# Optimization experiments

Hardware: AMD Instinct MI355X
Metric: run time of the kernel (lower is better)

## Reference

```python
import jax, jax.numpy as jnp
import numpy as np

VOCAB = 32000
EMB = 1024
SEQ = 2048
STACK = 8
N_HEADS = 16
ATTN = 64
BATCH = 2


def _ln(x, g, b, eps=1e-5):
    mu = jnp.mean(x, axis=-1, keepdims=True)
    var = jnp.var(x, axis=-1, keepdims=True)
    return (x - mu) * jax.lax.rsqrt(var + eps) * g + b


def setup_inputs() -> dict:
    key = jax.random.key(0)
    ks = jax.random.split(key, 16)
    s = lambda *sh: 0.02
    inp = {
        "x": jax.random.randint(ks[0], (BATCH, SEQ), 0, VOCAB),
        "emb": jax.random.normal(ks[1], (VOCAB, EMB), jnp.float32) * 0.02,
        # NOTE: one shared Attention_Head (all n_heads identical) and one shared Decoder (all stack layers identical)
        "Wq": jax.random.normal(ks[2], (EMB, ATTN), jnp.float32) * 0.02,
        "bq": jnp.zeros((ATTN,), jnp.float32),
        "Wk": jax.random.normal(ks[3], (EMB, ATTN), jnp.float32) * 0.02,
        "bk": jnp.zeros((ATTN,), jnp.float32),
        "Wv": jax.random.normal(ks[4], (EMB, ATTN), jnp.float32) * 0.02,
        "bv": jnp.zeros((ATTN,), jnp.float32),
        "Wd": jax.random.normal(ks[5], (ATTN * N_HEADS, EMB), jnp.float32) * 0.02,
        "bd": jnp.zeros((EMB,), jnp.float32),
        "g1": jnp.ones((EMB,), jnp.float32),
        "beta1": jnp.zeros((EMB,), jnp.float32),
        "g2": jnp.ones((EMB,), jnp.float32),
        "beta2": jnp.zeros((EMB,), jnp.float32),
        "W1": jax.random.normal(ks[6], (EMB, 4 * EMB), jnp.float32) * 0.02,
        "c1": jnp.zeros((4 * EMB,), jnp.float32),
        "W2": jax.random.normal(ks[7], (4 * EMB, EMB), jnp.float32) * 0.02,
        "c2": jnp.zeros((EMB,), jnp.float32),
        "Wfc": jax.random.normal(ks[8], (EMB, VOCAB), jnp.float32) * 0.02,
        "bfc": jnp.zeros((VOCAB,), jnp.float32),
    }
    return inp


def reference(x, emb, Wq, bq, Wk, bk, Wv, bv, Wd, bd, g1, beta1, g2, beta2, W1, c1, W2, c2, Wfc, bfc):
    h = emb[x]  # [B, S, E]
    scale = ATTN ** (-0.5)
    for _ in range(STACK):  # same (shared) decoder params every layer
        z = _ln(h, g1, beta1)
        q = z @ Wq + bq  # [B,S,A]
        k = z @ Wk + bk
        v = z @ Wv + bv
        # no causal mask applied in the original (tril buffer is unused)
        attn = jax.nn.softmax(jnp.einsum("bqa,bka->bqk", q, k) * scale, axis=-1)
        head = attn @ v  # [B,S,A]; all heads share weights -> identical outputs
        cat = jnp.tile(head, (1, 1, N_HEADS))  # [B,S,A*H]
        h = h + cat @ Wd + bd
        z2 = _ln(h, g2, beta2)
        h = h + jax.nn.relu(z2 @ W1 + c1) @ W2 + c2
    return h @ Wfc + bfc  # [B,S,VOCAB]
```

## Files before the change

kernel.cpp:

```cpp
#include <hip/hip_runtime.h>

typedef unsigned short u16;
typedef __attribute__((ext_vector_type(4))) float f32x4;
typedef __attribute__((ext_vector_type(8))) __bf16 bf16x8;
typedef __attribute__((ext_vector_type(4))) unsigned short u16x4;

static __device__ __forceinline__ u16 f2bf(float f) {
  union { float f; unsigned u; } v; v.f = f;
  unsigned r = v.u + 0x7fffu + ((v.u >> 16) & 1u);
  return (u16)(r >> 16);
}

#define GLD_LDS(g, l) __builtin_amdgcn_global_load_lds( \
    (const __attribute__((address_space(1))) void*)(g), \
    (__attribute__((address_space(3))) void*)(l), 16, 0, 0)

template<int EPI>
__global__ __launch_bounds__(512, 2)
void gemm8p(const u16* __restrict__ A, const u16* __restrict__ B,
            float* __restrict__ Cf, u16* __restrict__ Cb,
            const float* __restrict__ bias, float alpha,
            int K, int lda, int ldb, int ldc, int mtiles, int gm, int nsplit,
            long long sA, long long sB, long long sC)
{
  extern __shared__ u16 lds8[];
  const int t = threadIdx.x;
  const int w = t >> 6, l = t & 63;
  const int l15 = l & 15, l16 = l >> 4;
  const int wr = w >> 2, wc = w & 3;

  int wg = blockIdx.x;
  const int nwg = gridDim.x;
  {
    const int q = nwg >> 3, r = nwg & 7;
    const int xcd = wg & 7, loc = wg >> 3;
    wg = (xcd < r ? xcd * (q + 1) : r * (q + 1) + (xcd - r) * q) + loc;
  }
  const int ntiles = nwg / mtiles;
  const int gsz = gm * ntiles;
  const int gi = wg / gsz;
  const int rr = wg - gi * gsz;
  const int nt = rr / gm;
  const int mt = gi * gm + (rr - nt * gm);
  const int m0 = mt << 8, n0 = nt << 8;

  const int bz = blockIdx.z;
  int batch = bz, sp = 0;
  if (nsplit > 1) { batch = bz / nsplit; sp = bz - batch * nsplit; }
  const u16* Ab = A + (long long)batch * sA + (long long)sp * K;
  const u16* Bb = B + (long long)batch * sB + (long long)sp * K;
  const long long cbase = (long long)bz * sC;

  const int srow = t >> 3;
  const int scol = (((t & 7) ^ (srow & 7)) << 3);
  const u16* gA[4]; const u16* gB[4];
#pragma unroll
  for (int i = 0; i < 4; ++i) {
    gA[i] = Ab + (long long)(m0 + i * 64 + srow) * lda + scol;
    gB[i] = Bb + (long long)(n0 + i * 64 + srow) * ldb + scol;
  }
  const int ldst = w << 9;

  auto STAGE = [&](int buf) {
#pragma unroll
    for (int i = 0; i < 4; ++i) {
      GLD_LDS(gA[i], &lds8[buf * 16384 + i * 4096 + ldst]);
      gA[i] += 64;
    }
#pragma unroll
    for (int i = 0; i < 4; ++i) {
      GLD_LDS(gB[i], &lds8[32768 + buf * 16384 + i * 4096 + ldst]);
      gB[i] += 64;
    }
  };

  STAGE(0);
  STAGE(1);

  f32x4 acc[8][4] = {};
  const int nkt = K >> 6;
  const int aRow = wr * 128 + l15;
  const int bRow = wc * 64 + l15;
  const int swz = l15 & 7;

  for (int kt = 0; kt < nkt; ++kt) {
    const int buf = kt & 1;
    if (kt < nkt - 1) asm volatile("s_waitcnt vmcnt(8)" ::: "memory");
    else              asm volatile("s_waitcnt vmcnt(0)" ::: "memory");
    __builtin_amdgcn_s_barrier();
    __builtin_amdgcn_sched_barrier(0);

    const int abase = buf * 16384;
    const int bbase = 32768 + buf * 16384;
    bf16x8 af[4][2], bf[4][2];
#pragma unroll
    for (int mf = 0; mf < 4; ++mf)
#pragma unroll
      for (int kk = 0; kk < 2; ++kk)
        af[mf][kk] = *(const bf16x8*)&lds8[abase + (aRow + mf * 16) * 64 + ((((kk << 2) + l16)) ^ swz) * 8];
#pragma unroll
    for (int nf = 0; nf < 4; ++nf)
#pragma unroll
      for (int kk = 0; kk < 2; ++kk)
        bf[nf][kk] = *(const bf16x8*)&lds8[bbase + (bRow + nf * 16) * 64 + ((((kk << 2) + l16)) ^ swz) * 8];

    __builtin_amdgcn_s_setprio(1);
#pragma unroll
    for (int mf = 0; mf < 4; ++mf)
#pragma unroll
      for (int nf = 0; nf < 4; ++nf)
#pragma unroll
        for (int kk = 0; kk < 2; ++kk)
          acc[mf][nf] = __builtin_amdgcn_mfma_f32_16x16x32_bf16(af[mf][kk], bf[nf][kk], acc[mf][nf], 0, 0, 0);
    __builtin_amdgcn_s_setprio(0);

    bf16x8 ah[4][2];
#pragma unroll
    for (int mf = 0; mf < 4; ++mf)
#pragma unroll
      for (int kk = 0; kk < 2; ++kk)
        ah[mf][kk] = *(const bf16x8*)&lds8[abase + (aRow + 64 + mf * 16) * 64 + ((((kk << 2) + l16)) ^ swz) * 8];

    asm volatile("s_waitcnt lgkmcnt(0)" ::: "memory");
    __builtin_amdgcn_s_barrier();
    __builtin_amdgcn_sched_barrier(0);
    if (kt + 2 < nkt) STAGE(buf);

    __builtin_amdgcn_s_setprio(1);
#pragma unroll
    for (int mf = 0; mf < 4; ++mf)
#pragma unroll
      for (int nf = 0; nf < 4; ++nf)
#pragma unroll
        for (int kk = 0; kk < 2; ++kk)
          acc[mf + 4][nf] = __builtin_amdgcn_mfma_f32_16x16x32_bf16(ah[mf][kk], bf[nf][kk], acc[mf + 4][nf], 0, 0, 0);
    __builtin_amdgcn_s_setprio(0);
  }

#pragma unroll
  for (int mf = 0; mf < 8; ++mf) {
    const int rbase = m0 + wr * 128 + mf * 16 + l16 * 4;
#pragma unroll
    for (int nf = 0; nf < 4; ++nf) {
      const int col = n0 + wc * 64 + nf * 16 + l15;
      const float bv = bias ? bias[col] : 0.f;
#pragma unroll
      for (int r = 0; r < 4; ++r) {
        const long long idx = cbase + (long long)(rbase + r) * ldc + col;
        const float v = acc[mf][nf][r];
        if (EPI == 0)      Cf[idx] = alpha * v + bv;
        else if (EPI == 2) Cb[idx] = f2bf(v + bv);
        else               { float x = v + bv; Cb[idx] = f2bf(x > 0.f ? x : 0.f); }
      }
    }
  }
}

template<int EPI>
__global__ __launch_bounds__(256)
void gemm_bt(const u16* __restrict__ A, const u16* __restrict__ B,
             float* __restrict__ Cf, u16* __restrict__ Cb,
             const float* __restrict__ bias, float alpha,
             int K, int lda, int ldb, int ldc, int mtiles, int gm, int nsplit,
             long long sA, long long sB, long long sC)
{
  __shared__ u16 ldsA[128 * 32];
  __shared__ u16 ldsB[128 * 32];
  const int t = threadIdx.x;
  const int w = t >> 6, l = t & 63;

  int wg = blockIdx.x;
  const int nwg = gridDim.x;
  {
    const int q = nwg >> 3, r = nwg & 7;
    const int xcd = wg & 7, loc = wg >> 3;
    wg = (xcd < r ? xcd * (q + 1) : r * (q + 1) + (xcd - r) * q) + loc;
  }
  const int ntiles = nwg / mtiles;
  const int gsz = gm * ntiles;
  const int gi = wg / gsz;
  const int rr = wg - gi * gsz;
  const int nt = rr / gm;
  const int mt = gi * gm + (rr - nt * gm);
  const int m0 = mt << 7, n0 = nt << 7;

  const int bzRaw = blockIdx.z;
  int batch = bzRaw, sp = 0;
  if (nsplit > 1) { batch = bzRaw / nsplit; sp = bzRaw - batch * nsplit; }
  const u16* Ab = A + (long long)batch * sA + (long long)sp * K;
  const u16* Bb = B + (long long)batch * sB + (long long)sp * K;
  const long long cbase = (long long)bzRaw * sC;

  const int wr = (w >> 1) << 6, wc = (w & 1) << 6;
  const int l15 = l & 15, l16 = l >> 4;
  f32x4 acc[4][4] = {};

  for (int k0 = 0; k0 < K; k0 += 32) {
#pragma unroll
    for (int r = 0; r < 2; ++r) {
      const int o = (r << 12) + (t << 4);
      const int row = o >> 6;
      const int cole = (o & 63) >> 1;
      GLD_LDS(Ab + (long long)(m0 + row) * lda + k0 + cole, &ldsA[(r << 11) + (w << 9)]);
      GLD_LDS(Bb + (long long)(n0 + row) * ldb + k0 + cole, &ldsB[(r << 11) + (w << 9)]);
    }
    __syncthreads();
    bf16x8 af[4], bg[4];
#pragma unroll
    for (int i = 0; i < 4; ++i) {
      af[i] = *(const bf16x8*)&ldsA[(wr + i * 16 + l15) * 32 + l16 * 8];
      bg[i] = *(const bf16x8*)&ldsB[(wc + i * 16 + l15) * 32 + l16 * 8];
    }
#pragma unroll
    for (int i = 0; i < 4; ++i)
#pragma unroll
      for (int j = 0; j < 4; ++j)
        acc[i][j] = __builtin_amdgcn_mfma_f32_16x16x32_bf16(af[i], bg[j], acc[i][j], 0, 0, 0);
    __syncthreads();
  }

#pragma unroll
  for (int i = 0; i < 4; ++i) {
    const int rbase = m0 + wr + i * 16 + l16 * 4;
#pragma unroll
    for (int j = 0; j < 4; ++j) {
      const int col = n0 + wc + j * 16 + l15;
      const float bv = bias ? bias[col] : 0.f;
#pragma unroll
      for (int r = 0; r < 4; ++r) {
        const long long idx = cbase + (long long)(rbase + r) * ldc + col;
        const float v = acc[i][j][r];
        if (EPI == 0)      Cf[idx] = alpha * v + bv;
        else if (EPI == 1) Cf[idx] += v + bv;
        else if (EPI == 2) Cb[idx] = f2bf(v + bv);
        else               { float x = v + bv; Cb[idx] = f2bf(x > 0.f ? x : 0.f); }
      }
    }
  }
}

__device__ __forceinline__ void fstep(
    const bf16x8 (&ck)[4][2], const bf16x8 (&cv)[4][2],
    bf16x8 (&nk)[4][2], bf16x8 (&nv)[4][2],
    const bf16x8 (&qf)[2], float (&m)[4], float (&ls)[4], f32x4 (&o)[4],
    const u16* qb, const u16* vb, int kvn, u16* pl, int l15, int l16)
{
  f32x4 s[4] = {};
#pragma unroll
  for (int ni = 0; ni < 4; ++ni)
#pragma unroll
    for (int kk = 0; kk < 2; ++kk)
      s[ni] = __builtin_amdgcn_mfma_f32_16x16x32_bf16(qf[kk], ck[ni][kk], s[ni], 0, 0, 0);
#pragma unroll
  for (int ni = 0; ni < 4; ++ni)
#pragma unroll
    for (int kk = 0; kk < 2; ++kk)
      nk[ni][kk] = *(const bf16x8*)(qb + (kvn + ni * 16 + l15) * 256 + 64 + kk * 32 + l16 * 8);
#pragma unroll
  for (int ni = 0; ni < 4; ++ni) s[ni] *= 0.125f;
  float al[4], ps[4];
#pragma unroll
  for (int r = 0; r < 4; ++r) {
    float v = fmaxf(fmaxf(s[0][r], s[1][r]), fmaxf(s[2][r], s[3][r]));
    v = fmaxf(v, __shfl_xor(v, 1)); v = fmaxf(v, __shfl_xor(v, 2));
    v = fmaxf(v, __shfl_xor(v, 4)); v = fmaxf(v, __shfl_xor(v, 8));
    const float mn = fmaxf(m[r], v);
    al[r] = __expf(m[r] - mn);
    m[r] = mn;
    ps[r] = 0.f;
  }
#pragma unroll
  for (int ni = 0; ni < 4; ++ni)
#pragma unroll
    for (int r = 0; r < 4; ++r) {
      const float p = __expf(s[ni][r] - m[r]);
      ps[r] += p;
      pl[(l16 * 4 + r) * 72 + ni * 16 + l15] = f2bf(p);
    }
#pragma unroll
  for (int r = 0; r < 4; ++r) {
    float t = ps[r];
    t += __shfl_xor(t, 1); t += __shfl_xor(t, 2);
    t += __shfl_xor(t, 4); t += __shfl_xor(t, 8);
    ls[r] = ls[r] * al[r] + t;
  }
#pragma unroll
  for (int nd = 0; nd < 4; ++nd)
#pragma unroll
    for (int r = 0; r < 4; ++r) o[nd][r] *= al[r];
  bf16x8 pa[2];
#pragma unroll
  for (int kk = 0; kk < 2; ++kk)
    pa[kk] = *(const bf16x8*)&pl[l15 * 72 + kk * 32 + l16 * 8];
#pragma unroll
  for (int nd = 0; nd < 4; ++nd)
#pragma unroll
    for (int kk = 0; kk < 2; ++kk)
      o[nd] = __builtin_amdgcn_mfma_f32_16x16x32_bf16(pa[kk], cv[nd][kk], o[nd], 0, 0, 0);
#pragma unroll
  for (int nd = 0; nd < 4; ++nd)
#pragma unroll
    for (int kk = 0; kk < 2; ++kk)
      nv[nd][kk] = *(const bf16x8*)(vb + (nd * 16 + l15) * 2048 + kvn + kk * 32 + l16 * 8);
}

__global__ __launch_bounds__(256)
void flash4_k(const u16* __restrict__ qkv, const u16* __restrict__ vT,
              u16* __restrict__ head)
{
  __shared__ u16 plbuf[4][16 * 72];
  __shared__ float poL[4][16][64];
  __shared__ float pmL[4][16], plsL[4][16];
  const int t = threadIdx.x, sp = t >> 6, l = t & 63;
  const int l15 = l & 15, l16 = l >> 4;
  const int b = blockIdx.x >> 7, q0 = (blockIdx.x & 127) << 4;
  const int kvb = sp << 9;
  const u16* qb = qkv + (long long)b * 2048 * 256;
  const u16* vb = vT + (long long)b * 64 * 2048;
  u16* pl = &plbuf[sp][0];
  bf16x8 qf[2];
#pragma unroll
  for (int kk = 0; kk < 2; ++kk)
    qf[kk] = *(const bf16x8*)(qb + (q0 + l15) * 256 + kk * 32 + l16 * 8);
  float m[4], ls[4];
  f32x4 o[4] = {};
#pragma unroll
  for (int r = 0; r < 4; ++r) { m[r] = -1e30f; ls[r] = 0.f; }
  bf16x8 ka[4][2], va[4][2], kb[4][2], vb2[4][2];
#pragma unroll
  for (int ni = 0; ni < 4; ++ni)
#pragma unroll
    for (int kk = 0; kk < 2; ++kk) {
      ka[ni][kk] = *(const bf16x8*)(qb + (kvb + ni * 16 + l15) * 256 + 64 + kk * 32 + l16 * 8);
      va[ni][kk] = *(const bf16x8*)(vb + (ni * 16 + l15) * 2048 + kvb + kk * 32 + l16 * 8);
    }
  for (int ti = 0; ti < 8; ti += 2) {
    const int n1 = kvb + (ti + 1 < 8 ? (ti + 1) * 64 : 7 * 64);
    const int n2 = kvb + (ti + 2 < 8 ? (ti + 2) * 64 : 7 * 64);
    fstep(ka, va, kb, vb2, qf, m, ls, o, qb, vb, n1, pl, l15, l16);
    fstep(kb, vb2, ka, va, qf, m, ls, o, qb, vb, n2, pl, l15, l16);
  }
#pragma unroll
  for (int nd = 0; nd < 4; ++nd)
#pragma unroll
    for (int r = 0; r < 4; ++r)
      poL[sp][l16 * 4 + r][nd * 16 + l15] = o[nd][r];
  if (l15 == 0) {
#pragma unroll
    for (int r = 0; r < 4; ++r) {
      pmL[sp][l16 * 4 + r] = m[r];
      plsL[sp][l16 * 4 + r] = ls[r];
    }
  }
  __syncthreads();
#pragma unroll
  for (int i = 0; i < 4; ++i) {
    const int oi = t + i * 256;
    const int row = oi >> 6, col = oi & 63;
    float M = fmaxf(fmaxf(pmL[0][row], pmL[1][row]), fmaxf(pmL[2][row], pmL[3][row]));
    float L = 0.f, acc = 0.f;
#pragma unroll
    for (int s2 = 0; s2 < 4; ++s2) {
      const float e = __expf(pmL[s2][row] - M);
      L += plsL[s2][row] * e;
      acc += poL[s2][row][col] * e;
    }
    head[((long long)b * 2048 + q0 + row) * 64 + col] = f2bf(acc / L);
  }
}

__global__ __launch_bounds__(256)
void hwd_ln_k(const u16* __restrict__ head, const u16* __restrict__ Wdst,
              const float* __restrict__ bd, float* __restrict__ h,
              const float* __restrict__ g, const float* __restrict__ be,
              u16* __restrict__ z)
{
  const int t = threadIdx.x, w = t >> 6, l = t & 63;
  const int l15 = l & 15, l16 = l >> 4;
  const int r0 = blockIdx.x << 4;
  const int c0 = w << 8;
  bf16x8 af[2];
#pragma unroll
  for (int kk = 0; kk < 2; ++kk)
    af[kk] = *(const bf16x8*)&head[(long long)(r0 + l15) * 64 + kk * 32 + l16 * 8];
  f32x4 acc[16];
#pragma unroll
  for (int nf = 0; nf < 16; ++nf) {
    const int e = c0 + nf * 16 + l15;
    f32x4 a = {0.f, 0.f, 0.f, 0.f};
    bf16x8 b0 = *(const bf16x8*)&Wdst[e * 64 + l16 * 8];
    bf16x8 b1 = *(const bf16x8*)&Wdst[e * 64 + 32 + l16 * 8];
    a = __builtin_amdgcn_mfma_f32_16x16x32_bf16(af[0], b0, a, 0, 0, 0);
    a = __builtin_amdgcn_mfma_f32_16x16x32_bf16(af[1], b1, a, 0, 0, 0);
    acc[nf] = a;
  }
  float ps[4] = {0.f, 0.f, 0.f, 0.f}, pq[4] = {0.f, 0.f, 0.f, 0.f};
#pragma unroll
  for (int nf = 0; nf < 16; ++nf) {
    const int col = c0 + nf * 16 + l15;
#pragma unroll
    for (int r = 0; r < 4; ++r) {
      const long long row = r0 + l16 * 4 + r;
      float v = h[row * 1024 + col] + acc[nf][r] + bd[col];
      acc[nf][r] = v;
      ps[r] += v; pq[r] += v * v;
    }
  }
#pragma unroll
  for (int r = 0; r < 4; ++r) {
#pragma unroll
    for (int msk = 1; msk < 16; msk <<= 1) {
      ps[r] += __shfl_xor(ps[r], msk);
      pq[r] += __shfl_xor(pq[r], msk);
    }
  }
  __shared__ float S[4][16], Q[4][16];
  if (l15 == 0) {
#pragma unroll
    for (int r = 0; r < 4; ++r) { S[w][l16 * 4 + r] = ps[r]; Q[w][l16 * 4 + r] = pq[r]; }
  }
  __syncthreads();
  float mu[4], rstd[4];
#pragma unroll
  for (int r = 0; r < 4; ++r) {
    const int ri = l16 * 4 + r;
    const float s = S[0][ri] + S[1][ri] + S[2][ri] + S[3][ri];
    const float q = Q[0][ri] + Q[1][ri] + Q[2][ri] + Q[3][ri];
    mu[r] = s * (1.f / 1024.f);
    rstd[r] = rsqrtf(q * (1.f / 1024.f) - mu[r] * mu[r] + 1e-5f);
  }
#pragma unroll
  for (int nf = 0; nf < 16; ++nf) {
    const int col = c0 + nf * 16 + l15;
    const float gc = g[col], bc = be[col];
#pragma unroll
    for (int r = 0; r < 4; ++r) {
      const long long row = r0 + l16 * 4 + r;
      h[row * 1024 + col] = acc[nf][r];
      z[row * 1024 + col] = f2bf((acc[nf][r] - mu[r]) * rstd[r] * gc + bc);
    }
  }
}

__global__ __launch_bounds__(256)
void ln_k(const float* __restrict__ x, const float* __restrict__ g,
          const float* __restrict__ b, u16* __restrict__ z)
{
  const long long row = blockIdx.x;
  f32x4 v = ((const f32x4*)(x + row * 1024))[threadIdx.x];
  float s = v[0] + v[1] + v[2] + v[3];
  float q = v[0] * v[0] + v[1] * v[1] + v[2] * v[2] + v[3] * v[3];
#pragma unroll
  for (int o = 32; o; o >>= 1) { s += __shfl_down(s, o); q += __shfl_down(q, o); }
  __shared__ float rs_[4], rq_[4];
  const int l = threadIdx.x & 63, w = threadIdx.x >> 6;
  if (l == 0) { rs_[w] = s; rq_[w] = q; }
  __syncthreads();
  s = rs_[0] + rs_[1] + rs_[2] + rs_[3];
  q = rq_[0] + rq_[1] + rq_[2] + rq_[3];
  const float mu = s * (1.f / 1024.f);
  const float rstd = rsqrtf(q * (1.f / 1024.f) - mu * mu + 1e-5f);
  const f32x4 gv = ((const f32x4*)g)[threadIdx.x];
  const f32x4 bv = ((const f32x4*)b)[threadIdx.x];
  u16x4 o4;
#pragma unroll
  for (int e = 0; e < 4; ++e) o4[e] = f2bf((v[e] - mu) * rstd * gv[e] + bv[e]);
  ((u16x4*)(z + row * 1024))[threadIdx.x] = o4;
}

template<int MODE>
__global__ __launch_bounds__(256)
void reduce_ln_k(const u16* __restrict__ p, float* __restrict__ h,
                 const float* __restrict__ c2, const float* __restrict__ g,
                 const float* __restrict__ b, u16* __restrict__ z)
{
  const long long row = blockIdx.x;
  const int t = threadIdx.x;
  const long long i4 = (row << 8) + t;
  f32x4 v = ((const f32x4*)h)[i4] + ((const f32x4*)c2)[t];
#pragma unroll
  for (int s = 0; s < 4; ++s) {
    u16x4 pv = ((const u16x4*)p)[i4 + (long long)s * 1048576];
#pragma unroll
    for (int e = 0; e < 4; ++e) {
      union { unsigned u; float f; } x; x.u = ((unsigned)pv[e]) << 16;
      v[e] += x.f;
    }
  }
  u16x4 o4;
  if (MODE == 1) {
#pragma unroll
    for (int e = 0; e < 4; ++e) o4[e] = f2bf(v[e]);
  } else {
    ((f32x4*)h)[i4] = v;
    float s = v[0] + v[1] + v[2] + v[3];
    float q = v[0] * v[0] + v[1] * v[1] + v[2] * v[2] + v[3] * v[3];
#pragma unroll
    for (int o = 32; o; o >>= 1) { s += __shfl_down(s, o); q += __shfl_down(q, o); }
    __shared__ float rs_[4], rq_[4];
    const int l = t & 63, w = t >> 6;
    if (l == 0) { rs_[w] = s; rq_[w] = q; }
    __syncthreads();
    s = rs_[0] + rs_[1] + rs_[2] + rs_[3];
    q = rq_[0] + rq_[1] + rq_[2] + rq_[3];
    const float mu = s * (1.f / 1024.f);
    const float rstd = rsqrtf(q * (1.f / 1024.f) - mu * mu + 1e-5f);
    const f32x4 gv = ((const f32x4*)g)[t];
    const f32x4 bv = ((const f32x4*)b)[t];
#pragma unroll
    for (int e = 0; e < 4; ++e) o4[e] = f2bf((v[e] - mu) * rstd * gv[e] + bv[e]);
  }
  ((u16x4*)z)[i4] = o4;
}

__global__ __launch_bounds__(256)
void gather_k(const int* __restrict__ x, const float* __restrict__ emb, float* __restrict__ h)
{
  const long long tok = blockIdx.x;
  const long long r = (long long)x[tok] << 8;
  ((f32x4*)h)[(tok << 8) + threadIdx.x] = ((const f32x4*)emb)[r + threadIdx.x];
}

__global__ __launch_bounds__(256)
void tcast_k(const float* __restrict__ in, u16* __restrict__ out, int R, int C)
{
  __shared__ float tile[32][33];
  const int tx = threadIdx.x & 31, ty = threadIdx.x >> 5;
  const long long r0 = (long long)blockIdx.y << 5, c0 = (long long)blockIdx.x << 5;
#pragma unroll
  for (int yy = 0; yy < 32; yy += 8)
    tile[ty + yy][tx] = in[(r0 + ty + yy) * C + c0 + tx];
  __syncthreads();
#pragma unroll
  for (int yy = 0; yy < 32; yy += 8)
    out[(c0 + ty + yy) * R + r0 + tx] = f2bf(tile[tx][ty + yy]);
}

__global__ __launch_bounds__(256)
void wqkv_k(const float* __restrict__ Wq, const float* __restrict__ Wk,
            const float* __restrict__ Wv, u16* __restrict__ o)
{
  const int n = blockIdx.y;
  const long long e = (long long)blockIdx.x * 256 + threadIdx.x;
  float v = 0.f;
  if (n < 64)       v = Wq[e * 64 + n];
  else if (n < 128) v = Wk[e * 64 + (n - 64)];
  else if (n < 192) v = Wv[e * 64 + (n - 128)];
  o[(long long)n * 1024 + e] = f2bf(v);
}

__global__ __launch_bounds__(256)
void bqkv_k(const float* __restrict__ bq, const float* __restrict__ bk,
            const float* __restrict__ bv, float* __restrict__ o)
{
  const int n = threadIdx.x;
  float v = 0.f;
  if (n < 64)       v = bq[n];
  else if (n < 128) v = bk[n - 64];
  else if (n < 192) v = bv[n - 128];
  o[n] = v;
}

__global__ __launch_bounds__(256)
void wdsum_k(const float* __restrict__ Wd, u16* __restrict__ o)
{
  const int i = blockIdx.x * 256 + threadIdx.x;
  const int a = i & 63, e = i >> 6;
  float s = 0.f;
#pragma unroll
  for (int hh = 0; hh < 16; ++hh) s += Wd[(long long)(hh * 64 + a) * 1024 + e];
  o[i] = f2bf(s);
}

__global__ __launch_bounds__(256)
void reduce_qkv(const float* __restrict__ p, const float* __restrict__ bqkv,
                u16* __restrict__ qkv, u16* __restrict__ vT)
{
  const long long i4 = (long long)blockIdx.x * 256 + threadIdx.x;
  const int c4 = (int)(i4 & 63);
  const long long row = i4 >> 6;
  f32x4 s = ((const f32x4*)p)[i4] + ((const f32x4*)p)[i4 + 262144]
          + ((const f32x4*)bqkv)[c4];
  u16x4 o;
#pragma unroll
  for (int e = 0; e < 4; ++e) o[e] = f2bf(s[e]);
  ((u16x4*)qkv)[i4] = o;
  if (c4 >= 32 && c4 < 48) {
    const long long b = row >> 11, sidx = row & 2047;
#pragma unroll
    for (int e = 0; e < 4; ++e) {
      const int a = (c4 - 32) * 4 + e;
      vT[(b * 64 + a) * 2048 + sidx] = o[e];
    }
  }
}

extern "C" void kernel_launch(void* const* d_in, const int* in_sizes, int n_in,
                              void* d_out, int out_size, void* d_ws, size_t ws_size,
                              hipStream_t stream) {
  const int*   x   = (const int*)d_in[0];
  const float* emb = (const float*)d_in[1];
  const float* Wq  = (const float*)d_in[2];
  const float* bq  = (const float*)d_in[3];
  const float* Wk  = (const float*)d_in[4];
  const float* bk  = (const float*)d_in[5];
  const float* Wv  = (const float*)d_in[6];
  const float* bv  = (const float*)d_in[7];
  const float* Wd  = (const float*)d_in[8];
  const float* bd  = (const float*)d_in[9];
  const float* g1  = (const float*)d_in[10];
  const float* be1 = (const float*)d_in[11];
  const float* g2  = (const float*)d_in[12];
  const float* be2 = (const float*)d_in[13];
  const float* W1  = (const float*)d_in[14];
  const float* c1  = (const float*)d_in[15];
  const float* W2  = (const float*)d_in[16];
  const float* c2  = (const float*)d_in[17];
  const float* Wfc = (const float*)d_in[18];
  const float* bfc = (const float*)d_in[19];
  float* out = (float*)d_out;

  hipFuncSetAttribute(reinterpret_cast<const void*>(gemm8p<0>),
                      hipFuncAttributeMaxDynamicSharedMemorySize, 131072);
  hipFuncSetAttribute(reinterpret_cast<const void*>(gemm8p<2>),
                      hipFuncAttributeMaxDynamicSharedMemorySize, 131072);
  hipFuncSetAttribute(reinterpret_cast<const void*>(gemm8p<3>),
                      hipFuncAttributeMaxDynamicSharedMemorySize, 131072);

  char* ws = (char*)d_ws;
  size_t off = 0;
  auto alloc = [&](size_t bytes) { void* p = ws + off; off = (off + bytes + 255) & ~(size_t)255; return p; };
  float*  h     = (float*) alloc(4096ull * 1024 * 4);
  u16*    z     = (u16*)   alloc(4096ull * 1024 * 2);
  u16*    qkv   = (u16*)   alloc(4096ull * 256 * 2);
  u16*    vT    = (u16*)   alloc(2ull * 64 * 2048 * 2);
  u16*    head  = (u16*)   alloc(4096ull * 64 * 2);
  u16*    mid   = (u16*)   alloc(4096ull * 4096 * 2);
  char*   SCR   = (char*)  alloc(2ull * 4096 * 1024 * 4);
  float*  partQ = (float*)SCR;
  u16*    partF = (u16*)SCR;
  u16*    Wqkvt = (u16*)   alloc(256ull * 1024 * 2);
  float*  bqkv  = (float*) alloc(256 * 4);
  u16*    Wdst  = (u16*)   alloc(1024ull * 64 * 2);
  u16*    W1t   = (u16*)   alloc(4096ull * 1024 * 2);
  u16*    W2t   = (u16*)   alloc(1024ull * 4096 * 2);
  u16*    Wfct  = (u16*)   alloc(32000ull * 1024 * 2);

  gather_k<<<4096, 256, 0, stream>>>(x, emb, h);
  wqkv_k<<<dim3(4, 256), 256, 0, stream>>>(Wq, Wk, Wv, Wqkvt);
  bqkv_k<<<1, 256, 0, stream>>>(bq, bk, bv, bqkv);
  wdsum_k<<<256, 256, 0, stream>>>(Wd, Wdst);
  tcast_k<<<dim3(128, 32), 256, 0, stream>>>(W1, W1t, 1024, 4096);
  tcast_k<<<dim3(32, 128), 256, 0, stream>>>(W2, W2t, 4096, 1024);
  tcast_k<<<dim3(1000, 32), 256, 0, stream>>>(Wfc, Wfct, 1024, 32000);

  for (int layer = 0; layer < 8; ++layer) {
    if (layer == 0)
      ln_k<<<4096, 256, 0, stream>>>(h, g1, be1, z);
    gemm_bt<0><<<dim3(64, 1, 2), 256, 0, stream>>>(z, Wqkvt, partQ, nullptr, nullptr, 1.f,
        512, 1024, 1024, 256, 32, 32, 2, 0, 0, 1048576);
    reduce_qkv<<<1024, 256, 0, stream>>>(partQ, bqkv, qkv, vT);
    flash4_k<<<256, 256, 0, stream>>>(qkv, vT, head);
    hwd_ln_k<<<256, 256, 0, stream>>>(head, Wdst, bd, h, g2, be2, z);
    gemm8p<3><<<dim3(256, 1, 1), 512, 131072, stream>>>(z, W1t, nullptr, mid, c1, 1.f,
        1024, 1024, 1024, 4096, 16, 16, 1, 0, 0, 0);
    gemm8p<2><<<dim3(64, 1, 4), 512, 131072, stream>>>(mid, W2t, nullptr, partF, nullptr, 1.f,
        1024, 4096, 4096, 1024, 16, 16, 4, 0, 0, 4194304);
    if (layer < 7)
      reduce_ln_k<0><<<4096, 256, 0, stream>>>(partF, h, c2, g1, be1, z);
    else
      reduce_ln_k<1><<<4096, 256, 0, stream>>>(partF, h, c2, nullptr, nullptr, z);
  }
  gemm8p<0><<<dim3(2000, 1, 1), 512, 131072, stream>>>(z, Wfct, out, nullptr, bfc, 1.f,
      1024, 1024, 1024, 32000, 16, 8, 1, 0, 0, 0);
}
```

Before: 1.557 ms.

## Shrink GEMM K-tile to 32 with static LDS, store QKV split-K partials as bf16

The main 256x256 GEMM now stages K-slices of 32 instead of 64. That halves LDS per block to 64KB of static shared memory, which lets two 512-thread blocks fit per CU as the launch bounds request, and the swizzle is adjusted to the narrower rows. The cost is twice as many K iterations and barriers, with fewer MFMAs per barrier. Separately, the QKV split-K GEMM writes bf16 partials instead of fp32, halving that traffic at some cost in precision before the reduction.

```diff
diff --git a/kernel.cpp b/kernel.cpp
--- a/kernel.cpp
+++ b/kernel.cpp
@@ -10,6 +10,9 @@
   unsigned r = v.u + 0x7fffu + ((v.u >> 16) & 1u);
   return (u16)(r >> 16);
 }
+static __device__ __forceinline__ float bf2f(u16 u) {
+  union { unsigned u; float f; } x; x.u = ((unsigned)u) << 16; return x.f;
+}
 
 #define GLD_LDS(g, l) __builtin_amdgcn_global_load_lds( \
     (const __attribute__((address_space(1))) void*)(g), \
@@ -17,13 +20,13 @@
 
 template<int EPI>
 __global__ __launch_bounds__(512, 2)
-void gemm8p(const u16* __restrict__ A, const u16* __restrict__ B,
+void gemm2b(const u16* __restrict__ A, const u16* __restrict__ B,
             float* __restrict__ Cf, u16* __restrict__ Cb,
             const float* __restrict__ bias, float alpha,
             int K, int lda, int ldb, int ldc, int mtiles, int gm, int nsplit,
             long long sA, long long sB, long long sC)
 {
-  extern __shared__ u16 lds8[];
+  __shared__ u16 lds[32768];
   const int t = threadIdx.x;
   const int w = t >> 6, l = t & 63;
   const int l15 = l & 15, l16 = l >> 4;
@@ -51,89 +54,80 @@
   const u16* Bb = B + (long long)batch * sB + (long long)sp * K;
   const long long cbase = (long long)bz * sC;
 
-  const int srow = t >> 3;
-  const int scol = (((t & 7) ^ (srow & 7)) << 3);
-  const u16* gA[4]; const u16* gB[4];
-#pragma unroll
-  for (int i = 0; i < 4; ++i) {
-    gA[i] = Ab + (long long)(m0 + i * 64 + srow) * lda + scol;
-    gB[i] = Bb + (long long)(n0 + i * 64 + srow) * ldb + scol;
-  }
-  const int ldst = w << 9;
-
-  auto STAGE = [&](int buf) {
-#pragma unroll
-    for (int i = 0; i < 4; ++i) {
-      GLD_LDS(gA[i], &lds8[buf * 16384 + i * 4096 + ldst]);
-      gA[i] += 64;
-    }
-#pragma unroll
-    for (int i = 0; i < 4; ++i) {
-      GLD_LDS(gB[i], &lds8[32768 + buf * 16384 + i * 4096 + ldst]);
-      gB[i] += 64;
-    }
+  int srow[2], ssrc[2], sdst[2];
+#pragma unroll
+  for (int j = 0; j < 2; ++j) {
+    const int u = (j << 9) + (w << 6) + l;
+    srow[j] = u >> 2;
+    ssrc[j] = (((u & 3) ^ ((srow[j] >> 1) & 3)) << 3);
+    sdst[j] = ((j << 9) + (w << 6)) << 3;
+  }
+  auto STAGE = [&](int buf, int kt) {
+#pragma unroll
+    for (int j = 0; j < 2; ++j)
+      GLD_LDS(Ab + (long long)(m0 + srow[j]) * lda + kt * 32 + ssrc[j],
+              &lds[buf * 8192 + sdst[j]]);
+#pragma unroll
+    for (int j = 0; j < 2; ++j)
+      GLD_LDS(Bb + (long long)(n0 + srow[j]) * ldb + kt * 32 + ssrc[j],
+              &lds[16384 + buf * 8192 + sdst[j]]);
   };
 
-  STAGE(0);
-  STAGE(1);
+  const int nkt = K >> 5;
+  STAGE(0, 0);
+  if (nkt > 1) STAGE(1, 1);
 
   f32x4 acc[8][4] = {};
-  const int nkt = K >> 6;
   const int aRow = wr * 128 + l15;
   const int bRow = wc * 64 + l15;
-  const int swz = l15 & 7;
 
   for (int kt = 0; kt < nkt; ++kt) {
     const int buf = kt & 1;
-    if (kt < nkt - 1) asm volatile("s_waitcnt vmcnt(8)" ::: "memory");
+    if (kt < nkt - 1) asm volatile("s_waitcnt vmcnt(4)" ::: "memory");
     else              asm volatile("s_waitcnt vmcnt(0)" ::: "memory");
     __builtin_amdgcn_s_barrier();
     __builtin_amdgcn_sched_barrier(0);
 
-    const int abase = buf * 16384;
-    const int bbase = 32768 + buf * 16384;
-    bf16x8 af[4][2], bf[4][2];
+    const int abase = buf * 8192;
+    const int bbase = 16384 + buf * 8192;
+    bf16x8 af[4], bg[4];
+#pragma unroll
+    for (int mf = 0; mf < 4; ++mf) {
+      const int r2 = aRow + mf * 16;
+      af[mf] = *(const bf16x8*)&lds[abase + r2 * 32 + ((l16 ^ ((r2 >> 1) & 3)) << 3)];
+    }
+#pragma unroll
+    for (int nf = 0; nf < 4; ++nf) {
+      const int r2 = bRow + nf * 16;
+      bg[nf] = *(const bf16x8*)&lds[bbase + r2 * 32 + ((l16 ^ ((r2 >> 1) & 3)) << 3)];
+    }
+
+    __builtin_amdgcn_s_setprio(1);
 #pragma unroll
     for (int mf = 0; mf < 4; ++mf)
 #pragma unroll
-      for (int kk = 0; kk < 2; ++kk)
-        af[mf][kk] = *(const bf16x8*)&lds8[abase + (aRow + mf * 16) * 64 + ((((kk << 2) + l16)) ^ swz) * 8];
-#pragma unroll
-    for (int nf = 0; nf < 4; ++nf)
-#pragma unroll
-      for (int kk = 0; kk < 2; ++kk)
-        bf[nf][kk] = *(const bf16x8*)&lds8[bbase + (bRow + nf * 16) * 64 + ((((kk << 2) + l16)) ^ swz) * 8];
-
-    __builtin_amdgcn_s_setprio(1);
-#pragma unroll
-    for (int mf = 0; mf < 4; ++mf)
-#pragma unroll
       for (int nf = 0; nf < 4; ++nf)
-#pragma unroll
-        for (int kk = 0; kk < 2; ++kk)
-          acc[mf][nf] = __builtin_amdgcn_mfma_f32_16x16x32_bf16(af[mf][kk], bf[nf][kk], acc[mf][nf], 0, 0, 0);
+        acc[mf][nf] = __builtin_amdgcn_mfma_f32_16x16x32_bf16(af[mf], bg[nf], acc[mf][nf], 0, 0, 0);
     __builtin_amdgcn_s_setprio(0);
 
-    bf16x8 ah[4][2];
-#pragma unroll
-    for (int mf = 0; mf < 4; ++mf)
-#pragma unroll
-      for (int kk = 0; kk < 2; ++kk)
-        ah[mf][kk] = *(const bf16x8*)&lds8[abase + (aRow + 64 + mf * 16) * 64 + ((((kk << 2) + l16)) ^ swz) * 8];
+    bf16x8 ah[4];
+#pragma unroll
+    for (int mf = 0; mf < 4; ++mf) {
+      const int r2 = aRow + 64 + mf * 16;
+      ah[mf] = *(const bf16x8*)&lds[abase + r2 * 32 + ((l16 ^ ((r2 >> 1) & 3)) << 3)];
+    }
 
     asm volatile("s_waitcnt lgkmcnt(0)" ::: "memory");
     __builtin_amdgcn_s_barrier();
     __builtin_amdgcn_sched_barrier(0);
-    if (kt + 2 < nkt) STAGE(buf);
+    if (kt + 2 < nkt) STAGE(buf, kt + 2);
 
     __builtin_amdgcn_s_setprio(1);
 #pragma unroll
     for (int mf = 0; mf < 4; ++mf)
 #pragma unroll
       for (int nf = 0; nf < 4; ++nf)
-#pragma unroll
-        for (int kk = 0; kk < 2; ++kk)
-          acc[mf + 4][nf] = __builtin_amdgcn_mfma_f32_16x16x32_bf16(ah[mf][kk], bf[nf][kk], acc[mf + 4][nf], 0, 0, 0);
+        acc[mf + 4][nf] = __builtin_amdgcn_mfma_f32_16x16x32_bf16(ah[mf], bg[nf], acc[mf + 4][nf], 0, 0, 0);
     __builtin_amdgcn_s_setprio(0);
   }
 
@@ -482,10 +476,7 @@
   for (int s = 0; s < 4; ++s) {
     u16x4 pv = ((const u16x4*)p)[i4 + (long long)s * 1048576];
 #pragma unroll
-    for (int e = 0; e < 4; ++e) {
-      union { unsigned u; float f; } x; x.u = ((unsigned)pv[e]) << 16;
-      v[e] += x.f;
-    }
+    for (int e = 0; e < 4; ++e) v[e] += bf2f(pv[e]);
   }
   u16x4 o4;
   if (MODE == 1) {
@@ -573,24 +564,25 @@
 }
 
 __global__ __launch_bounds__(256)
-void reduce_qkv(const float* __restrict__ p, const float* __restrict__ bqkv,
+void reduce_qkv(const u16* __restrict__ p, const float* __restrict__ bqkv,
                 u16* __restrict__ qkv, u16* __restrict__ vT)
 {
   const long long i4 = (long long)blockIdx.x * 256 + threadIdx.x;
   const int c4 = (int)(i4 & 63);
   const long long row = i4 >> 6;
-  f32x4 s = ((const f32x4*)p)[i4] + ((const f32x4*)p)[i4 + 262144]
-          + ((const f32x4*)bqkv)[c4];
+  u16x4 a = ((const u16x4*)p)[i4];
+  u16x4 b2 = ((const u16x4*)p)[i4 + 262144];
+  const f32x4 bb = ((const f32x4*)bqkv)[c4];
   u16x4 o;
 #pragma unroll
-  for (int e = 0; e < 4; ++e) o[e] = f2bf(s[e]);
+  for (int e = 0; e < 4; ++e) o[e] = f2bf(bf2f(a[e]) + bf2f(b2[e]) + bb[e]);
   ((u16x4*)qkv)[i4] = o;
   if (c4 >= 32 && c4 < 48) {
     const long long b = row >> 11, sidx = row & 2047;
 #pragma unroll
     for (int e = 0; e < 4; ++e) {
-      const int a = (c4 - 32) * 4 + e;
-      vT[(b * 64 + a) * 2048 + sidx] = o[e];
+      const int aa = (c4 - 32) * 4 + e;
+      vT[(b * 64 + aa) * 2048 + sidx] = o[e];
     }
   }
 }
@@ -620,13 +612,6 @@
   const float* bfc = (const float*)d_in[19];
   float* out = (float*)d_out;
 
-  hipFuncSetAttribute(reinterpret_cast<const void*>(gemm8p<0>),
-                      hipFuncAttributeMaxDynamicSharedMemorySize, 131072);
-  hipFuncSetAttribute(reinterpret_cast<const void*>(gemm8p<2>),
-                      hipFuncAttributeMaxDynamicSharedMemorySize, 131072);
-  hipFuncSetAttribute(reinterpret_cast<const void*>(gemm8p<3>),
-                      hipFuncAttributeMaxDynamicSharedMemorySize, 131072);
-
   char* ws = (char*)d_ws;
   size_t off = 0;
   auto alloc = [&](size_t bytes) { void* p = ws + off; off = (off + bytes + 255) & ~(size_t)255; return p; };
@@ -637,7 +622,7 @@
   u16*    head  = (u16*)   alloc(4096ull * 64 * 2);
   u16*    mid   = (u16*)   alloc(4096ull * 4096 * 2);
   char*   SCR   = (char*)  alloc(2ull * 4096 * 1024 * 4);
-  float*  partQ = (float*)SCR;
+  u16*    partQb= (u16*)SCR;
   u16*    partF = (u16*)SCR;
   u16*    Wqkvt = (u16*)   alloc(256ull * 1024 * 2);
   float*  bqkv  = (float*) alloc(256 * 4);
@@ -657,20 +642,20 @@
   for (int layer = 0; layer < 8; ++layer) {
     if (layer == 0)
       ln_k<<<4096, 256, 0, stream>>>(h, g1, be1, z);
-    gemm_bt<0><<<dim3(64, 1, 2), 256, 0, stream>>>(z, Wqkvt, partQ, nullptr, nullptr, 1.f,
+    gemm_bt<2><<<dim3(64, 1, 2), 256, 0, stream>>>(z, Wqkvt, nullptr, partQb, nullptr, 1.f,
         512, 1024, 1024, 256, 32, 32, 2, 0, 0, 1048576);
-    reduce_qkv<<<1024, 256, 0, stream>>>(partQ, bqkv, qkv, vT);
+    reduce_qkv<<<1024, 256, 0, stream>>>(partQb, bqkv, qkv, vT);
     flash4_k<<<256, 256, 0, stream>>>(qkv, vT, head);
     hwd_ln_k<<<256, 256, 0, stream>>>(head, Wdst, bd, h, g2, be2, z);
-    gemm8p<3><<<dim3(256, 1, 1), 512, 131072, stream>>>(z, W1t, nullptr, mid, c1, 1.f,
+    gemm2b<3><<<dim3(256, 1, 1), 512, 0, stream>>>(z, W1t, nullptr, mid, c1, 1.f,
         1024, 1024, 1024, 4096, 16, 16, 1, 0, 0, 0);
-    gemm8p<2><<<dim3(64, 1, 4), 512, 131072, stream>>>(mid, W2t, nullptr, partF, nullptr, 1.f,
+    gemm2b<2><<<dim3(64, 1, 4), 512, 0, stream>>>(mid, W2t, nullptr, partF, nullptr, 1.f,
         1024, 4096, 4096, 1024, 16, 16, 4, 0, 0, 4194304);
     if (layer < 7)
       reduce_ln_k<0><<<4096, 256, 0, stream>>>(partF, h, c2, g1, be1, z);
     else
       reduce_ln_k<1><<<4096, 256, 0, stream>>>(partF, h, c2, nullptr, nullptr, z);
   }
-  gemm8p<0><<<dim3(2000, 1, 1), 512, 131072, stream>>>(z, Wfct, out, nullptr, bfc, 1.f,
+  gemm2b<0><<<dim3(2000, 1, 1), 512, 0, stream>>>(z, Wfct, out, nullptr, bfc, 1.f,
       1024, 1024, 1024, 32000, 16, 8, 1, 0, 0, 0);
 }
```

Result: slower. 1.634 ms (+4.9%).
